# Kernel tuning notes

Measured on AMD Instinct MI355X. Metric: run time of the kernel, lower is better.

Reference implementation:

```python
import jax, jax.numpy as jnp
import numpy as np

N, E = 50000, 800000
HID, EDIM, HEADS = 256, 64, 8
C = HID // HEADS  # per-head channels = 32
NEG_SLOPE = 0.2
LN_EPS = 1e-5


def setup_inputs() -> dict:
    key = jax.random.key(0)
    ks = jax.random.split(key, 12)
    s = 1.0 / np.sqrt(HID)
    se = 1.0 / np.sqrt(EDIM)
    return {
        "x": jax.random.normal(ks[0], (N, HID), jnp.float32),
        "edge_index": jax.random.randint(ks[1], (2, E), 0, N, jnp.int32),
        "edge_attr": jax.random.normal(ks[2], (E, EDIM), jnp.float32),
        "W": jax.random.uniform(ks[3], (HID, HEADS * C), jnp.float32, -s, s),
        "W_e": jax.random.uniform(ks[4], (EDIM, HEADS * C), jnp.float32, -se, se),
        "att_src": jax.random.normal(ks[5], (HEADS, C), jnp.float32) * 0.1,
        "att_dst": jax.random.normal(ks[6], (HEADS, C), jnp.float32) * 0.1,
        "att_edge": jax.random.normal(ks[7], (HEADS, C), jnp.float32) * 0.1,
        "bias": jnp.zeros((HEADS * C,), jnp.float32),
        "gamma": jnp.ones((HID,), jnp.float32),
        "beta": jnp.zeros((HID,), jnp.float32),
    }


def _gat_block(x, edge_index, edge_attr, W, W_e, att_src, att_dst, att_edge, bias, gamma, beta):
    n = x.shape[0]
    src, dst = edge_index[0], edge_index[1]
    # node projection (shared for src/dst, as in PyG GATConv non-bipartite)
    xp = (x @ W).reshape(n, HEADS, C)                       # [N,H,C]
    a_src = jnp.einsum("nhc,hc->nh", xp, att_src)          # [N,H]
    a_dst = jnp.einsum("nhc,hc->nh", xp, att_dst)          # [N,H]
    ep = (edge_attr @ W_e).reshape(-1, HEADS, C)            # [E,H,C]
    a_edge = jnp.einsum("ehc,hc->eh", ep, att_edge)        # [E,H]
    # per-edge attention logit + LeakyReLU
    alpha = a_src[src] + a_dst[dst] + a_edge                # [E,H]
    alpha = jax.nn.leaky_relu(alpha, NEG_SLOPE)
    # segment softmax over incoming edges of each dst node
    m = jax.ops.segment_max(alpha, dst, num_segments=n)     # [N,H]
    m = jnp.where(jnp.isfinite(m), m, 0.0)
    ea = jnp.exp(alpha - m[dst])
    den = jax.ops.segment_sum(ea, dst, num_segments=n)      # [N,H]
    attn = ea / (den[dst] + 1e-16)                          # [E,H]
    # weighted message + scatter-add
    msg = xp[src] * attn[:, :, None]                        # [E,H,C]
    out = jax.ops.segment_sum(msg, dst, num_segments=n)     # [N,H,C]
    h = out.reshape(n, HEADS * C) + bias
    # residual + LayerNorm (dropout in eval mode -> identity)
    y = x + h
    mu = jnp.mean(y, axis=-1, keepdims=True)
    var = jnp.var(y, axis=-1, keepdims=True)
    return (y - mu) * jax.lax.rsqrt(var + LN_EPS) * gamma + beta


def reference(x, edge_index, edge_attr, W, W_e, att_src, att_dst, att_edge, bias, gamma, beta):
    return _gat_block(x, edge_index, edge_attr, W, W_e, att_src, att_dst, att_edge, bias, gamma, beta)
```

## Files before the change

kernel.cpp:

```cpp
#include <hip/hip_runtime.h>
#include <cstdint>

#define NEG_SLOPE 0.2f
#define LN_EPS 1e-5f

typedef __bf16 bf16x8 __attribute__((ext_vector_type(8)));
typedef float f32x4 __attribute__((ext_vector_type(4)));

__device__ __forceinline__ float b2f(unsigned int u) {
    union { unsigned int i; float f; } x; x.i = u << 16; return x.f;
}
__device__ __forceinline__ unsigned short f2b(float f) {
    union { float f; unsigned int i; } x; x.f = f;
    unsigned int r = x.i + 0x7fffu + ((x.i >> 16) & 1u);
    return (unsigned short)(r >> 16);
}

__global__ void k0a_prep(const float* __restrict__ W,
                         const float* __restrict__ We,
                         const float* __restrict__ att_src,
                         const float* __restrict__ att_dst,
                         const float* __restrict__ att_edge,
                         float* __restrict__ u_src, float* __restrict__ u_dst,
                         float* __restrict__ vW) {
    int t = threadIdx.x;
    const float* wr = W + t * 256;
    for (int h = 0; h < 8; h++) {
        float s1 = 0.f, s2 = 0.f;
        for (int c = 0; c < 32; c++) {
            float w = wr[h * 32 + c];
            s1 += w * att_src[h * 32 + c];
            s2 += w * att_dst[h * 32 + c];
        }
        u_src[t * 8 + h] = s1; u_dst[t * 8 + h] = s2;
    }
    if (t < 64) {
        const float* er = We + t * 256;
        for (int h = 0; h < 8; h++) {
            float s = 0.f;
            for (int c = 0; c < 32; c++) s += er[h * 32 + c] * att_edge[h * 32 + c];
            vW[t * 8 + h] = s;
        }
    }
}

__global__ void k0b_wfrag(const float* __restrict__ W,
                          unsigned short* __restrict__ Wf) {
    int T = blockIdx.x * 256 + threadIdx.x;
    int j    = T & 7;
    int lane = (T >> 3) & 63;
    int kk   = (T >> 9) & 7;
    int i    = (T >> 12) & 3;
    int w    = T >> 14;
    int n = w * 64 + i * 16 + (lane & 15);
    int k = kk * 32 + (lane >> 4) * 8 + j;
    Wf[T] = f2b(W[k * 256 + n]);
}

__global__ __launch_bounds__(256) void k1_xp(const float* __restrict__ x,
                                             const unsigned short* __restrict__ Wf,
                                             const float* __restrict__ u_src,
                                             const float* __restrict__ u_dst,
                                             unsigned short* __restrict__ xp,
                                             float* __restrict__ a_src,
                                             float* __restrict__ a_dst, int N) {
    __shared__ float red[2][4][16][8];
    int m0 = blockIdx.x * 16;
    int lane = threadIdx.x & 63, wave = threadIdx.x >> 6;
    int quad = lane >> 4, l16 = lane & 15;
    int mrow = m0 + l16; if (mrow > N - 1) mrow = N - 1;
    const float* ap = x + (size_t)mrow * 256 + quad * 8;
    const unsigned short* wfw = Wf + (size_t)wave * 16384;
    f32x4 ac0 = {0,0,0,0}, ac1 = {0,0,0,0}, ac2 = {0,0,0,0}, ac3 = {0,0,0,0};
    float pas[8] = {0,0,0,0,0,0,0,0}, pad_[8] = {0,0,0,0,0,0,0,0};
#pragma unroll
    for (int kk = 0; kk < 8; kk++) {
        float4 fa0 = *(const float4*)(ap + kk * 32);
        float4 fa1 = *(const float4*)(ap + kk * 32 + 4);
        if ((kk >> 1) == wave) {
            float f[8] = {fa0.x, fa0.y, fa0.z, fa0.w, fa1.x, fa1.y, fa1.z, fa1.w};
#pragma unroll
            for (int j = 0; j < 8; j++) {
                int k = kk * 32 + quad * 8 + j;
                const float4* up = (const float4*)(u_src + k * 8);
                float4 s0 = up[0], s1 = up[1];
                const float4* vp = (const float4*)(u_dst + k * 8);
                float4 d0 = vp[0], d1 = vp[1];
                pas[0] += f[j] * s0.x; pas[1] += f[j] * s0.y;
                pas[2] += f[j] * s0.z; pas[3] += f[j] * s0.w;
                pas[4] += f[j] * s1.x; pas[5] += f[j] * s1.y;
                pas[6] += f[j] * s1.z; pas[7] += f[j] * s1.w;
                pad_[0] += f[j] * d0.x; pad_[1] += f[j] * d0.y;
                pad_[2] += f[j] * d0.z; pad_[3] += f[j] * d0.w;
                pad_[4] += f[j] * d1.x; pad_[5] += f[j] * d1.y;
                pad_[6] += f[j] * d1.z; pad_[7] += f[j] * d1.w;
            }
        }
        union { unsigned short u[8]; bf16x8 v; } A;
        A.u[0] = f2b(fa0.x); A.u[1] = f2b(fa0.y); A.u[2] = f2b(fa0.z); A.u[3] = f2b(fa0.w);
        A.u[4] = f2b(fa1.x); A.u[5] = f2b(fa1.y); A.u[6] = f2b(fa1.z); A.u[7] = f2b(fa1.w);
        const unsigned short* wk = wfw + kk * 512 + lane * 8;
        bf16x8 b0 = *(const bf16x8*)(wk);
        bf16x8 b1 = *(const bf16x8*)(wk + 4096);
        bf16x8 b2 = *(const bf16x8*)(wk + 8192);
        bf16x8 b3 = *(const bf16x8*)(wk + 12288);
        ac0 = __builtin_amdgcn_mfma_f32_16x16x32_bf16(A.v, b0, ac0, 0, 0, 0);
        ac1 = __builtin_amdgcn_mfma_f32_16x16x32_bf16(A.v, b1, ac1, 0, 0, 0);
        ac2 = __builtin_amdgcn_mfma_f32_16x16x32_bf16(A.v, b2, ac2, 0, 0, 0);
        ac3 = __builtin_amdgcn_mfma_f32_16x16x32_bf16(A.v, b3, ac3, 0, 0, 0);
    }
#pragma unroll
    for (int h = 0; h < 8; h++) {
        pas[h] += __shfl_xor(pas[h], 16, 64);
        pas[h] += __shfl_xor(pas[h], 32, 64);
        pad_[h] += __shfl_xor(pad_[h], 16, 64);
        pad_[h] += __shfl_xor(pad_[h], 32, 64);
    }
    if (quad == 0) {
#pragma unroll
        for (int h = 0; h < 8; h++) {
            red[0][wave][l16][h] = pas[h];
            red[1][wave][l16][h] = pad_[h];
        }
    }
    int nb = wave * 64;
#pragma unroll
    for (int r = 0; r < 4; r++) {
        int m = m0 + quad * 4 + r;
        if (m < N) {
            unsigned short* op = xp + (size_t)m * 256 + nb + l16;
            op[0]  = f2b(ac0[r]); op[16] = f2b(ac1[r]);
            op[32] = f2b(ac2[r]); op[48] = f2b(ac3[r]);
        }
    }
    __syncthreads();
    {
        int t = threadIdx.x;
        int arr = t >> 7, r = (t >> 3) & 15, h = t & 7;
        int m = m0 + r;
        if (m < N) {
            float sum = red[arr][0][r][h] + red[arr][1][r][h]
                      + red[arr][2][r][h] + red[arr][3][r][h];
            (arr ? a_dst : a_src)[m * 8 + h] = sum;
        }
    }
}

__global__ __launch_bounds__(256) void k2_edge(const int* __restrict__ ei,
                                               const float* __restrict__ eattr,
                                               const float* __restrict__ vW,
                                               const float* __restrict__ a_src,
                                               const float* __restrict__ a_dst,
                                               unsigned short* __restrict__ ea,
                                               int* __restrict__ deg, int E) {
    __shared__ float sv[2048];
    int t = threadIdx.x;
    if (t < 128) {
        const float4* g = (const float4*)vW;
        float4* s4 = (float4*)sv;
        int k = t >> 1, half = t & 1;
        int kl = ((k & 15) << 2) | (k >> 4);
        s4[kl * 2 + half] = g[t];
    }
    __syncthreads();
    int e = blockIdx.x * 64 + (t >> 2), kp = t & 3;
    if (e >= E) return;
    const float4* ar = (const float4*)(eattr + (size_t)e * 64 + kp * 16);
    float acc[8] = {0,0,0,0,0,0,0,0};
#pragma unroll
    for (int q = 0; q < 4; q++) {
        float4 u = ar[q];
        float f[4] = {u.x, u.y, u.z, u.w};
#pragma unroll
        for (int j = 0; j < 4; j++) {
            int kl = ((q * 4 + j) << 2) | kp;
            const float4* vp = (const float4*)(sv + kl * 8);
            float4 v0 = vp[0], v1 = vp[1];
            acc[0] += f[j] * v0.x; acc[1] += f[j] * v0.y;
            acc[2] += f[j] * v0.z; acc[3] += f[j] * v0.w;
            acc[4] += f[j] * v1.x; acc[5] += f[j] * v1.y;
            acc[6] += f[j] * v1.z; acc[7] += f[j] * v1.w;
        }
    }
#pragma unroll
    for (int h = 0; h < 8; h++) {
        acc[h] += __shfl_xor(acc[h], 1, 64);
        acc[h] += __shfl_xor(acc[h], 2, 64);
    }
    int s = ei[e], d = ei[E + e];
    float2 asv = *(const float2*)(a_src + s * 8 + kp * 2);
    float2 adv = *(const float2*)(a_dst + d * 8 + kp * 2);
    float l0 = asv.x + adv.x + acc[kp * 2];
    float l1 = asv.y + adv.y + acc[kp * 2 + 1];
    l0 = (l0 > 0.f) ? l0 : NEG_SLOPE * l0;
    l1 = (l1 > 0.f) ? l1 : NEG_SLOPE * l1;
    unsigned int pk = (unsigned)f2b(__expf(l0)) | ((unsigned)f2b(__expf(l1)) << 16);
    ((unsigned int*)ea)[(size_t)e * 4 + kp] = pk;
    if (kp == 0) atomicAdd(deg + d, 1);
}

__global__ __launch_bounds__(1024) void k3a_scan(const int* __restrict__ deg,
                                                 int* __restrict__ rowptr,
                                                 int* __restrict__ bsum, int N) {
    __shared__ int s[1024];
    int t = threadIdx.x, i = blockIdx.x * 1024 + t;
    int v = (i < N) ? deg[i] : 0;
    s[t] = v; __syncthreads();
    for (int off = 1; off < 1024; off <<= 1) {
        int add = (t >= off) ? s[t - off] : 0;
        __syncthreads();
        s[t] += add;
        __syncthreads();
    }
    if (i < N) rowptr[i] = s[t] - v;
    if (t == 1023) bsum[blockIdx.x] = s[1023];
}
__global__ void k3b_scan(const int* __restrict__ bsum, int* __restrict__ boff, int nb) {
    int l = threadIdx.x;
    int v = (l < nb) ? bsum[l] : 0;
    int x = v;
#pragma unroll
    for (int off = 1; off < 64; off <<= 1) {
        int y = __shfl_up(x, off, 64);
        if (l >= off) x += y;
    }
    if (l < nb) boff[l] = x - v;
}
__global__ __launch_bounds__(1024) void k3c_add(int* __restrict__ rowptr,
                                                int* __restrict__ cursor,
                                                const int* __restrict__ boff, int N, int E) {
    int i = blockIdx.x * 1024 + threadIdx.x;
    if (i < N) {
        int r = rowptr[i] + boff[blockIdx.x];
        rowptr[i] = r; cursor[i] = r;
    }
    if (i == 0) rowptr[N] = E;
}
__global__ __launch_bounds__(256) void k3d_scatter(const int* __restrict__ ei,
                                                   int* __restrict__ cursor,
                                                   int* __restrict__ perm, int E) {
    int e = blockIdx.x * 256 + threadIdx.x;
    if (e >= E) return;
    int d = ei[E + e];
    int p = atomicAdd(cursor + d, 1);
    perm[p] = e;
}

__global__ __launch_bounds__(256) void k4_agg(const float* __restrict__ xin,
                                              const unsigned short* __restrict__ xp,
                                              const unsigned short* __restrict__ ea,
                                              const int* __restrict__ rowptr,
                                              const int* __restrict__ perm,
                                              const int* __restrict__ ei,
                                              const float* __restrict__ bias,
                                              const float* __restrict__ gamma,
                                              const float* __restrict__ beta,
                                              float* __restrict__ out, int N) {
    __shared__ int ssrc[64];
    __shared__ float sea[64 * 9];
    __shared__ float racc[4][64][4];
    __shared__ float rden[8];
    int n = blockIdx.x;
    int t = threadIdx.x, wave = t >> 6, l = t & 63;
    int start = rowptr[n], end = rowptr[n + 1];
    int hh = l >> 3;
    float a0 = 0.f, a1 = 0.f, a2 = 0.f, a3 = 0.f;
    float den[8] = {0,0,0,0,0,0,0,0};
    for (int base = start; base < end; base += 64) {
        int cnt = end - base; if (cnt > 64) cnt = 64;
        if (t < cnt) {
            int e = perm[base + t];
            ssrc[t] = ei[e];
            uint4 u = ((const uint4*)ea)[e];
            float v0 = b2f(u.x & 0xffffu), v1 = b2f(u.x >> 16);
            float v2 = b2f(u.y & 0xffffu), v3 = b2f(u.y >> 16);
            float v4 = b2f(u.z & 0xffffu), v5 = b2f(u.z >> 16);
            float v6 = b2f(u.w & 0xffffu), v7 = b2f(u.w >> 16);
            float* sp = sea + t * 9;
            sp[0] = v0; sp[1] = v1; sp[2] = v2; sp[3] = v3;
            sp[4] = v4; sp[5] = v5; sp[6] = v6; sp[7] = v7;
            den[0] += v0; den[1] += v1; den[2] += v2; den[3] += v3;
            den[4] += v4; den[5] += v5; den[6] += v6; den[7] += v7;
        }
        __syncthreads();
        for (int i = wave; i < cnt; i += 4) {
            int s = ssrc[i];
            uint2 u = *(const uint2*)(xp + (size_t)s * 256 + l * 4);
            float w = sea[i * 9 + hh];
            a0 += b2f(u.x & 0xffffu) * w; a1 += b2f(u.x >> 16) * w;
            a2 += b2f(u.y & 0xffffu) * w; a3 += b2f(u.y >> 16) * w;
        }
        __syncthreads();
    }
    racc[wave][l][0] = a0; racc[wave][l][1] = a1;
    racc[wave][l][2] = a2; racc[wave][l][3] = a3;
    if (wave == 0) {
#pragma unroll
        for (int off = 32; off > 0; off >>= 1) {
#pragma unroll
            for (int j = 0; j < 8; j++) den[j] += __shfl_xor(den[j], off, 64);
        }
        if (l < 8) rden[l] = den[l];
    }
    __syncthreads();
    if (wave != 0) return;
    float m0 = racc[0][l][0] + racc[1][l][0] + racc[2][l][0] + racc[3][l][0];
    float m1 = racc[0][l][1] + racc[1][l][1] + racc[2][l][1] + racc[3][l][1];
    float m2 = racc[0][l][2] + racc[1][l][2] + racc[2][l][2] + racc[3][l][2];
    float m3 = racc[0][l][3] + racc[1][l][3] + racc[2][l][3] + racc[3][l][3];
    float sinv = 1.0f / (rden[hh] + 1e-16f);
    m0 *= sinv; m1 *= sinv; m2 *= sinv; m3 *= sinv;
    float4 xv = *(const float4*)(xin + (size_t)n * 256 + l * 4);
    float4 bv = *(const float4*)(bias + l * 4);
    float y0 = xv.x + m0 + bv.x;
    float y1 = xv.y + m1 + bv.y;
    float y2 = xv.z + m2 + bv.z;
    float y3 = xv.w + m3 + bv.w;
    float s1 = y0 + y1 + y2 + y3;
    float s2 = y0 * y0 + y1 * y1 + y2 * y2 + y3 * y3;
#pragma unroll
    for (int o = 32; o > 0; o >>= 1) {
        s1 += __shfl_down(s1, o, 64);
        s2 += __shfl_down(s2, o, 64);
    }
    s1 = __shfl(s1, 0, 64); s2 = __shfl(s2, 0, 64);
    float mu = s1 * (1.f / 256.f);
    float var = s2 * (1.f / 256.f) - mu * mu;
    float rs = rsqrtf(var + LN_EPS);
    float4 gv  = *(const float4*)(gamma + l * 4);
    float4 btv = *(const float4*)(beta + l * 4);
    float4 ov;
    ov.x = (y0 - mu) * rs * gv.x + btv.x;
    ov.y = (y1 - mu) * rs * gv.y + btv.y;
    ov.z = (y2 - mu) * rs * gv.z + btv.z;
    ov.w = (y3 - mu) * rs * gv.w + btv.w;
    *(float4*)(out + (size_t)n * 256 + l * 4) = ov;
}

extern "C" void kernel_launch(void* const* d_in, const int* in_sizes, int n_in,
                              void* d_out, int out_size, void* d_ws, size_t ws_size,
                              hipStream_t stream) {
    const float* x     = (const float*)d_in[0];
    const int*   ei    = (const int*)d_in[1];
    const float* eattr = (const float*)d_in[2];
    const float* W     = (const float*)d_in[3];
    const float* We    = (const float*)d_in[4];
    const float* atts  = (const float*)d_in[5];
    const float* attd  = (const float*)d_in[6];
    const float* atte  = (const float*)d_in[7];
    const float* bias  = (const float*)d_in[8];
    const float* gamma = (const float*)d_in[9];
    const float* beta  = (const float*)d_in[10];
    float* out = (float*)d_out;
    int N = in_sizes[0] / 256;
    int E = in_sizes[1] / 2;

    char* p = (char*)d_ws;
    auto carve = [&](size_t bytes) -> void* {
        void* r = (void*)p; p += (bytes + 255) & ~(size_t)255; return r;
    };
    unsigned short* xp = (unsigned short*)carve((size_t)N * 256 * 2);
    unsigned short* ea = (unsigned short*)carve((size_t)E * 8 * 2);
    float* a_src       = (float*)carve((size_t)N * 8 * 4);
    float* a_dst       = (float*)carve((size_t)N * 8 * 4);
    int*   deg         = (int*)carve((size_t)N * 4);
    int*   rowptr      = (int*)carve((size_t)(N + 1) * 4);
    int*   cursor      = (int*)carve((size_t)N * 4);
    int*   perm        = (int*)carve((size_t)E * 4);
    int*   bsum        = (int*)carve(1024);
    int*   boff        = (int*)carve(1024);
    float* u_src       = (float*)carve(2048 * 4);
    float* u_dst       = (float*)carve(2048 * 4);
    float* vW          = (float*)carve(512 * 4);
    unsigned short* Wf = (unsigned short*)carve(65536 * 2);

    hipMemsetAsync(deg, 0, (size_t)N * 4, stream);

    hipLaunchKernelGGL(k0a_prep, dim3(1), dim3(256), 0, stream,
                       W, We, atts, attd, atte, u_src, u_dst, vW);
    hipLaunchKernelGGL(k0b_wfrag, dim3(256), dim3(256), 0, stream, W, Wf);
    hipLaunchKernelGGL(k1_xp, dim3((N + 15) / 16), dim3(256), 0, stream,
                       x, Wf, u_src, u_dst, xp, a_src, a_dst, N);
    hipLaunchKernelGGL(k2_edge, dim3((E + 63) / 64), dim3(256), 0, stream,
                       ei, eattr, vW, a_src, a_dst, ea, deg, E);
    int nb = (N + 1023) / 1024;
    hipLaunchKernelGGL(k3a_scan, dim3(nb), dim3(1024), 0, stream, deg, rowptr, bsum, N);
    hipLaunchKernelGGL(k3b_scan, dim3(1), dim3(64), 0, stream, bsum, boff, nb);
    hipLaunchKernelGGL(k3c_add, dim3(nb), dim3(1024), 0, stream, rowptr, cursor, boff, N, E);
    hipLaunchKernelGGL(k3d_scatter, dim3((E + 255) / 256), dim3(256), 0, stream,
                       ei, cursor, perm, E);
    hipLaunchKernelGGL(k4_agg, dim3(N), dim3(256), 0, stream,
                       x, xp, ea, rowptr, perm, ei, bias, gamma, beta, out, N);
}
```

Baseline: 622.5 us.

## Build CSR first and write edge weights and sources directly in dst-sorted order

Degree counting and the prefix scan now run before the edge kernel. The edge kernel then claims a CSR slot with an atomic and writes the exp-logits and source index straight into dst-sorted arrays. This drops the separate perm scatter kernel and the indirect perm/ei/ea gathers in aggregation, which now reads contiguously, at the cost of scattered writes in the edge kernel. The aggregation loop is also unrolled by 4 and 2 so several xp gathers are in flight per wave.

Measured after the change: 610.6 us. No clear change (-1.9%).

```diff
diff --git a/kernel.cpp b/kernel.cpp
--- a/kernel.cpp
+++ b/kernel.cpp
@@ -55,6 +55,12 @@
     int n = w * 64 + i * 16 + (lane & 15);
     int k = kk * 32 + (lane >> 4) * 8 + j;
     Wf[T] = f2b(W[k * 256 + n]);
+}
+
+__global__ __launch_bounds__(256) void k_deg(const int* __restrict__ ei,
+                                             int* __restrict__ deg, int E) {
+    int e = blockIdx.x * 256 + threadIdx.x;
+    if (e < E) atomicAdd(deg + ei[E + e], 1);
 }
 
 __global__ __launch_bounds__(256) void k1_xp(const float* __restrict__ x,
@@ -151,8 +157,9 @@
                                                const float* __restrict__ vW,
                                                const float* __restrict__ a_src,
                                                const float* __restrict__ a_dst,
-                                               unsigned short* __restrict__ ea,
-                                               int* __restrict__ deg, int E) {
+                                               int* __restrict__ cursor,
+                                               int* __restrict__ srcs,
+                                               uint4* __restrict__ eav, int E) {
     __shared__ float sv[2048];
     int t = threadIdx.x;
     if (t < 128) {
@@ -195,8 +202,12 @@
     l0 = (l0 > 0.f) ? l0 : NEG_SLOPE * l0;
     l1 = (l1 > 0.f) ? l1 : NEG_SLOPE * l1;
     unsigned int pk = (unsigned)f2b(__expf(l0)) | ((unsigned)f2b(__expf(l1)) << 16);
-    ((unsigned int*)ea)[(size_t)e * 4 + kp] = pk;
-    if (kp == 0) atomicAdd(deg + d, 1);
+    int l = t & 63;
+    int p = 0;
+    if (kp == 0) p = atomicAdd(cursor + d, 1);
+    p = __shfl(p, l & 60, 64);
+    ((unsigned int*)eav)[(size_t)p * 4 + kp] = pk;
+    if (kp == 0) srcs[p] = s;
 }
 
 __global__ __launch_bounds__(1024) void k3a_scan(const int* __restrict__ deg,
@@ -236,22 +247,12 @@
     }
     if (i == 0) rowptr[N] = E;
 }
-__global__ __launch_bounds__(256) void k3d_scatter(const int* __restrict__ ei,
-                                                   int* __restrict__ cursor,
-                                                   int* __restrict__ perm, int E) {
-    int e = blockIdx.x * 256 + threadIdx.x;
-    if (e >= E) return;
-    int d = ei[E + e];
-    int p = atomicAdd(cursor + d, 1);
-    perm[p] = e;
-}
 
 __global__ __launch_bounds__(256) void k4_agg(const float* __restrict__ xin,
                                               const unsigned short* __restrict__ xp,
-                                              const unsigned short* __restrict__ ea,
+                                              const int* __restrict__ srcs,
+                                              const uint4* __restrict__ eav,
                                               const int* __restrict__ rowptr,
-                                              const int* __restrict__ perm,
-                                              const int* __restrict__ ei,
                                               const float* __restrict__ bias,
                                               const float* __restrict__ gamma,
                                               const float* __restrict__ beta,
@@ -269,9 +270,8 @@
     for (int base = start; base < end; base += 64) {
         int cnt = end - base; if (cnt > 64) cnt = 64;
         if (t < cnt) {
-            int e = perm[base + t];
-            ssrc[t] = ei[e];
-            uint4 u = ((const uint4*)ea)[e];
+            ssrc[t] = srcs[base + t];
+            uint4 u = eav[base + t];
             float v0 = b2f(u.x & 0xffffu), v1 = b2f(u.x >> 16);
             float v2 = b2f(u.y & 0xffffu), v3 = b2f(u.y >> 16);
             float v4 = b2f(u.z & 0xffffu), v5 = b2f(u.z >> 16);
@@ -283,12 +283,40 @@
             den[4] += v4; den[5] += v5; den[6] += v6; den[7] += v7;
         }
         __syncthreads();
-        for (int i = wave; i < cnt; i += 4) {
-            int s = ssrc[i];
-            uint2 u = *(const uint2*)(xp + (size_t)s * 256 + l * 4);
-            float w = sea[i * 9 + hh];
-            a0 += b2f(u.x & 0xffffu) * w; a1 += b2f(u.x >> 16) * w;
-            a2 += b2f(u.y & 0xffffu) * w; a3 += b2f(u.y >> 16) * w;
+        int i = wave;
+        for (; i + 12 < cnt; i += 16) {
+            int s0 = ssrc[i], s1 = ssrc[i + 4], s2 = ssrc[i + 8], s3 = ssrc[i + 12];
+            uint2 u0 = *(const uint2*)(xp + (size_t)s0 * 256 + l * 4);
+            uint2 u1 = *(const uint2*)(xp + (size_t)s1 * 256 + l * 4);
+            uint2 u2 = *(const uint2*)(xp + (size_t)s2 * 256 + l * 4);
+            uint2 u3 = *(const uint2*)(xp + (size_t)s3 * 256 + l * 4);
+            float w0 = sea[i * 9 + hh],        w1 = sea[(i + 4) * 9 + hh];
+            float w2 = sea[(i + 8) * 9 + hh],  w3 = sea[(i + 12) * 9 + hh];
+            a0 += b2f(u0.x & 0xffffu) * w0; a1 += b2f(u0.x >> 16) * w0;
+            a2 += b2f(u0.y & 0xffffu) * w0; a3 += b2f(u0.y >> 16) * w0;
+            a0 += b2f(u1.x & 0xffffu) * w1; a1 += b2f(u1.x >> 16) * w1;
+            a2 += b2f(u1.y & 0xffffu) * w1; a3 += b2f(u1.y >> 16) * w1;
+            a0 += b2f(u2.x & 0xffffu) * w2; a1 += b2f(u2.x >> 16) * w2;
+            a2 += b2f(u2.y & 0xffffu) * w2; a3 += b2f(u2.y >> 16) * w2;
+            a0 += b2f(u3.x & 0xffffu) * w3; a1 += b2f(u3.x >> 16) * w3;
+            a2 += b2f(u3.y & 0xffffu) * w3; a3 += b2f(u3.y >> 16) * w3;
+        }
+        for (; i + 4 < cnt; i += 8) {
+            int s0 = ssrc[i], s1 = ssrc[i + 4];
+            uint2 u0 = *(const uint2*)(xp + (size_t)s0 * 256 + l * 4);
+            uint2 u1 = *(const uint2*)(xp + (size_t)s1 * 256 + l * 4);
+            float w0 = sea[i * 9 + hh], w1 = sea[(i + 4) * 9 + hh];
+            a0 += b2f(u0.x & 0xffffu) * w0; a1 += b2f(u0.x >> 16) * w0;
+            a2 += b2f(u0.y & 0xffffu) * w0; a3 += b2f(u0.y >> 16) * w0;
+            a0 += b2f(u1.x & 0xffffu) * w1; a1 += b2f(u1.x >> 16) * w1;
+            a2 += b2f(u1.y & 0xffffu) * w1; a3 += b2f(u1.y >> 16) * w1;
+        }
+        for (; i < cnt; i += 4) {
+            int s0 = ssrc[i];
+            uint2 u0 = *(const uint2*)(xp + (size_t)s0 * 256 + l * 4);
+            float w0 = sea[i * 9 + hh];
+            a0 += b2f(u0.x & 0xffffu) * w0; a1 += b2f(u0.x >> 16) * w0;
+            a2 += b2f(u0.y & 0xffffu) * w0; a3 += b2f(u0.y >> 16) * w0;
         }
         __syncthreads();
     }
@@ -360,13 +388,13 @@
         void* r = (void*)p; p += (bytes + 255) & ~(size_t)255; return r;
     };
     unsigned short* xp = (unsigned short*)carve((size_t)N * 256 * 2);
-    unsigned short* ea = (unsigned short*)carve((size_t)E * 8 * 2);
+    uint4* eav         = (uint4*)carve((size_t)E * 16);
+    int*   srcs        = (int*)carve((size_t)E * 4);
     float* a_src       = (float*)carve((size_t)N * 8 * 4);
     float* a_dst       = (float*)carve((size_t)N * 8 * 4);
     int*   deg         = (int*)carve((size_t)N * 4);
     int*   rowptr      = (int*)carve((size_t)(N + 1) * 4);
     int*   cursor      = (int*)carve((size_t)N * 4);
-    int*   perm        = (int*)carve((size_t)E * 4);
     int*   bsum        = (int*)carve(1024);
     int*   boff        = (int*)carve(1024);
     float* u_src       = (float*)carve(2048 * 4);
@@ -379,16 +407,15 @@
     hipLaunchKernelGGL(k0a_prep, dim3(1), dim3(256), 0, stream,
                        W, We, atts, attd, atte, u_src, u_dst, vW);
     hipLaunchKernelGGL(k0b_wfrag, dim3(256), dim3(256), 0, stream, W, Wf);
-    hipLaunchKernelGGL(k1_xp, dim3((N + 15) / 16), dim3(256), 0, stream,
-                       x, Wf, u_src, u_dst, xp, a_src, a_dst, N);
-    hipLaunchKernelGGL(k2_edge, dim3((E + 63) / 64), dim3(256), 0, stream,
-                       ei, eattr, vW, a_src, a_dst, ea, deg, E);
+    hipLaunchKernelGGL(k_deg, dim3((E + 255) / 256), dim3(256), 0, stream, ei, deg, E);
     int nb = (N + 1023) / 1024;
     hipLaunchKernelGGL(k3a_scan, dim3(nb), dim3(1024), 0, stream, deg, rowptr, bsum, N);
     hipLaunchKernelGGL(k3b_scan, dim3(1), dim3(64), 0, stream, bsum, boff, nb);
     hipLaunchKernelGGL(k3c_add, dim3(nb), dim3(1024), 0, stream, rowptr, cursor, boff, N, E);
-    hipLaunchKernelGGL(k3d_scatter, dim3((E + 255) / 256), dim3(256), 0, stream,
-                       ei, cursor, perm, E);
+    hipLaunchKernelGGL(k1_xp, dim3((N + 15) / 16), dim3(256), 0, stream,
+                       x, Wf, u_src, u_dst, xp, a_src, a_dst, N);
+    hipLaunchKernelGGL(k2_edge, dim3((E + 63) / 64), dim3(256), 0, stream,
+                       ei, eattr, vW, a_src, a_dst, cursor, srcs, eav, E);
     hipLaunchKernelGGL(k4_agg, dim3(N), dim3(256), 0, stream,
-                       x, xp, ea, rowptr, perm, ei, bias, gamma, beta, out, N);
-}
+                       x, xp, srcs, eav, rowptr, bias, gamma, beta, out, N);
+}
```
